# Kernel tuning notes

Measured on AMD Instinct MI355X. Metric: run time of the kernel, lower is better.

Reference implementation:

```python
import jax, jax.numpy as jnp
import numpy as np

B, C, H, W = 4, 256, 128, 128
HEADS = 8
EPS_LN = 1e-5
EPS_NORM = 1e-12


def conv2d(x, w, padding, groups=1):
    return jax.lax.conv_general_dilated(
        x, w, window_strides=(1, 1), padding=padding,
        feature_group_count=groups,
        dimension_numbers=('NCHW', 'OIHW', 'NCHW'))


def layernorm_c(x, weight, bias):
    # WithBias LayerNorm over channel dim (to_3d makes channels the last axis)
    mu = jnp.mean(x, axis=1, keepdims=True)
    var = jnp.var(x, axis=1, keepdims=True)
    xn = (x - mu) / jnp.sqrt(var + EPS_LN)
    return xn * weight[None, :, None, None] + bias[None, :, None, None]


def setup_inputs() -> dict:
    key = jax.random.key(0)
    ks = jax.random.split(key, 8)
    s = 0.02
    return {
        'x': jax.random.normal(ks[0], (B, C, H, W), jnp.float32),
        'y': jax.random.normal(ks[1], (B, C, H, W), jnp.float32),
        'ln_kv_w': jnp.ones((C,), jnp.float32),
        'ln_kv_b': jnp.zeros((C,), jnp.float32),
        'ln_q_w': jnp.ones((C,), jnp.float32),
        'ln_q_b': jnp.zeros((C,), jnp.float32),
        'W_kv': jax.random.normal(ks[2], (2 * C, C, 1, 1), jnp.float32) * s,
        'W_dw': jax.random.normal(ks[3], (2 * C, 1, 3, 3), jnp.float32) * s,
        'W_q': jax.random.normal(ks[4], (C, C, 3, 3), jnp.float32) * s,
        'W_proj': jax.random.normal(ks[5], (C, C, 1, 1), jnp.float32) * s,
        'temperature': jnp.ones((HEADS, 1, 1), jnp.float32),
    }


def reference(x, y, ln_kv_w, ln_kv_b, ln_q_w, ln_q_b, W_kv, W_dw, W_q, W_proj, temperature):
    b, c, h, w = x.shape
    xn = layernorm_c(x, ln_kv_w, ln_kv_b)
    yn = layernorm_c(y, ln_q_w, ln_q_b)

    # Attention (MDTA channel cross-attention)
    kv = conv2d(xn, W_kv, 'VALID')                       # [b, 2c, h, w]
    kv = conv2d(kv, W_dw, 'SAME', groups=2 * c)          # depthwise 3x3
    k, v = jnp.split(kv, 2, axis=1)
    q = conv2d(yn, W_q, 'SAME')                          # [b, c, h, w]

    def heads(t):
        return t.reshape(b, HEADS, c // HEADS, h * w)    # [b, head, ch, hw]

    q, k, v = heads(q), heads(k), heads(v)
    q = q / jnp.maximum(jnp.linalg.norm(q, axis=-1, keepdims=True), EPS_NORM)
    k = k / jnp.maximum(jnp.linalg.norm(k, axis=-1, keepdims=True), EPS_NORM)

    attn = jnp.einsum('bhcn,bhdn->bhcd', q, k) * temperature[None]
    attn = jax.nn.softmax(attn, axis=-1)
    out = jnp.einsum('bhcd,bhdn->bhcn', attn, v)         # [b, head, ch, hw]
    out = out.reshape(b, c, h, w)
    out = conv2d(out, W_proj, 'VALID')
    return yn + out
```

## Files before the change

kernel.cpp:

```cpp
#include <hip/hip_runtime.h>
#include <hip/hip_bf16.h>

typedef __hip_bfloat16 bf16;
typedef __attribute__((ext_vector_type(8))) short bf16x8;
typedef __attribute__((ext_vector_type(4))) float f32x4;

#define Bn 4
#define Cn 256
#define C2n 512
#define Hn 128
#define Wn 128
#define HWn 16384
#define HEADSn 8
#define CHn 32
#define PADW 132
#define PADH 130
#define PROW (PADW * Cn)
#define PBn ((size_t)PADH * PROW)

static __device__ __forceinline__ float b2f(bf16 v) { return __bfloat162float(v); }
static __device__ __forceinline__ bf16 f2b(float v) { return __float2bfloat16(v); }
static __device__ __forceinline__ short f2bs(float v) {
    bf16 t = f2b(v);
    return __builtin_bit_cast(short, t);
}
static __device__ __forceinline__ float s2f(short s) {
    bf16 t = __builtin_bit_cast(bf16, s);
    return b2f(t);
}

static __device__ __forceinline__ void gload16(const void* g, void* l) {
    __builtin_amdgcn_global_load_lds(
        (const __attribute__((address_space(1))) unsigned int*)g,
        (__attribute__((address_space(3))) unsigned int*)l,
        16, 0, 0);
}


__global__ void cast_kernel(const float* __restrict__ src, bf16* __restrict__ dst, int n) {
    for (int i = blockIdx.x * 256 + threadIdx.x; i < n; i += gridDim.x * 256)
        dst[i] = f2b(src[i]);
}

__global__ void wq_repack_kernel(const float* __restrict__ Wq, bf16* __restrict__ wr) {
    int i = blockIdx.x * 256 + threadIdx.x;
    if (i < Cn * Cn) {
        int oc = i >> 8, c = i & 255;
        #pragma unroll
        for (int dy = 0; dy < 3; dy++)
            #pragma unroll
            for (int dx = 0; dx < 3; dx++)
                wr[((size_t)dy * Cn + oc) * 768 + dx * Cn + c] =
                    f2b(Wq[(size_t)i * 9 + dy * 3 + dx]);
    }
}

__global__ void halo_zero_kernel(bf16* __restrict__ yp) {
    int yq = blockIdx.x;
    int b  = blockIdx.y;
    bf16* row = yp + (size_t)b * PBn + (size_t)yq * PROW;
    bf16x8 z = {0, 0, 0, 0, 0, 0, 0, 0};
    if (yq == 0 || yq == PADH - 1) {
        for (int i = threadIdx.x; i < PROW / 8; i += 256)
            *(bf16x8*)&row[(size_t)i * 8] = z;
    } else {
        for (int i = threadIdx.x; i < 128; i += 256) {
            if (i < 32) *(bf16x8*)&row[(size_t)i * 8] = z;
            else        *(bf16x8*)&row[(size_t)129 * Cn + (size_t)(i - 32) * 8] = z;
        }
    }
}

__global__ void ln_stats_kernel(const float* __restrict__ x,
                                const float* __restrict__ y,
                                float* __restrict__ stats) {
    int which = blockIdx.y;
    const float* src = which ? y : x;
    int pix = blockIdx.x * 256 + threadIdx.x;
    int b = pix >> 14;
    int hw = pix & (HWn - 1);
    const float* xb = src + (size_t)b * Cn * HWn + hw;
    float s = 0.f, ss = 0.f;
    for (int c = 0; c < Cn; c++) {
        float v = xb[(size_t)c * HWn];
        s += v; ss += v * v;
    }
    float mu  = s * (1.f / Cn);
    float var = ss * (1.f / Cn) - mu * mu;
    float inv = rsqrtf(var + 1e-5f);
    float* st = stats + (size_t)which * 2 * Bn * HWn;
    st[pix] = mu;
    st[(size_t)Bn * HWn + pix] = inv;
}

__global__ void transpose_ln_kernel(const float* __restrict__ src,
                                    const float* __restrict__ stats,
                                    const float* __restrict__ gw,
                                    const float* __restrict__ gb,
                                    bf16* __restrict__ dst, int pad) {
    __shared__ float t[64][65];
    __shared__ float swv[64], sbv[64], smu[64], sinv[64];
    int tid = threadIdx.x;
    int pxt = blockIdx.x;
    int ct  = blockIdx.y;
    int b   = blockIdx.z;
    int p0  = pxt * 64;
    if (tid < 64)       { swv[tid] = gw[ct * 64 + tid]; sbv[tid] = gb[ct * 64 + tid]; }
    else if (tid < 128) { int p = tid - 64;  smu[p]  = stats[(size_t)b * HWn + p0 + p]; }
    else if (tid < 192) { int p = tid - 128; sinv[p] = stats[(size_t)Bn * HWn + (size_t)b * HWn + p0 + p]; }
    const float* sb_ = src + ((size_t)b * Cn + ct * 64) * HWn + p0;
    for (int i = tid; i < 1024; i += 256) {
        int r = i >> 4, sg = (i & 15) * 4;
        float4 v = *(const float4*)&sb_[(size_t)r * HWn + sg];
        t[r][sg + 0] = v.x; t[r][sg + 1] = v.y; t[r][sg + 2] = v.z; t[r][sg + 3] = v.w;
    }
    __syncthreads();
    size_t base;
    if (pad) {
        int yr = p0 >> 7, x0 = p0 & 127;
        base = (size_t)b * PBn + ((size_t)(yr + 1) * PADW + (x0 + 1)) * Cn + ct * 64;
    } else {
        base = ((size_t)b * HWn + p0) * Cn + ct * 64;
    }
    for (int i = tid; i < 512; i += 256) {
        int p = i >> 3, cg = (i & 7) * 8;
        float mu = smu[p], inv = sinv[p];
        bf16x8 v;
        #pragma unroll
        for (int j = 0; j < 8; j++) {
            float val = (t[cg + j][p] - mu) * inv * swv[cg + j] + sbv[cg + j];
            v[j] = f2bs(val);
        }
        *(bf16x8*)&dst[base + (size_t)p * Cn + cg] = v;
    }
}

__global__ __launch_bounds__(256) void kv1x1_mfma_kernel(
        const bf16* __restrict__ xn_pm,
        const bf16* __restrict__ wkv_pk,
        bf16* __restrict__ kv) {
    __shared__ __attribute__((aligned(16))) short Als[8192];
    __shared__ __attribute__((aligned(16))) short Bls[8192];
    int tid  = threadIdx.x;
    int px0  = blockIdx.x * 128;
    int oc0  = blockIdx.y * 128;
    int b    = blockIdx.z;
    int wave = tid >> 6, lane = tid & 63;
    int lm = lane & 15, kq = lane >> 4;
    int l7 = lm & 7;

    f32x4 acc[2][8];
    #pragma unroll
    for (int mt = 0; mt < 2; mt++)
        #pragma unroll
        for (int nt = 0; nt < 8; nt++) acc[mt][nt] = (f32x4){0.f, 0.f, 0.f, 0.f};

    int rA = tid >> 3;
    int cA = (tid & 7) ^ (rA & 7);
    const short* pA = (const short*)wkv_pk + ((size_t)(oc0 + rA)) * Cn + cA * 8;
    const short* pB = (const short*)xn_pm + ((size_t)b * HWn + px0 + rA) * Cn + cA * 8;
    short* lA = &Als[wave * 512];
    short* lB = &Bls[wave * 512];

    for (int kc = 0; kc < Cn; kc += 64) {
        __syncthreads();
        #pragma unroll
        for (int j = 0; j < 4; j++) {
            gload16(pA + kc + j * (32 * Cn), lA + j * 2048);
            gload16(pB + kc + j * (32 * Cn), lB + j * 2048);
        }
        __syncthreads();
        #pragma unroll
        for (int kk = 0; kk < 2; kk++) {
            int xo = (((kk << 2) | kq) ^ l7) * 8;
            bf16x8 afr[2], bfr[8];
            #pragma unroll
            for (int mt = 0; mt < 2; mt++)
                afr[mt] = *(const bf16x8*)&Als[(wave * 32 + mt * 16 + lm) * 64 + xo];
            #pragma unroll
            for (int nt = 0; nt < 8; nt++)
                bfr[nt] = *(const bf16x8*)&Bls[(nt * 16 + lm) * 64 + xo];
            #pragma unroll
            for (int mt = 0; mt < 2; mt++)
                #pragma unroll
                for (int nt = 0; nt < 8; nt++)
                    acc[mt][nt] = __builtin_amdgcn_mfma_f32_16x16x32_bf16(
                        afr[mt], bfr[nt], acc[mt][nt], 0, 0, 0);
        }
    }
    bf16* kb = kv + ((size_t)b * C2n + oc0) * HWn + px0;
    #pragma unroll
    for (int mt = 0; mt < 2; mt++) {
        int ocl = wave * 32 + mt * 16 + kq * 4;
        #pragma unroll
        for (int nt = 0; nt < 8; nt++) {
            int pxx = nt * 16 + lm;
            #pragma unroll
            for (int r = 0; r < 4; r++)
                kb[(size_t)(ocl + r) * HWn + pxx] = f2b(acc[mt][nt][r]);
        }
    }
}

__global__ void dw_kernel(const bf16* __restrict__ kv,
                          const float* __restrict__ Wdw,
                          bf16* __restrict__ kvdw) {
    __shared__ float st[18][132];
    int tid = threadIdx.x;
    int r0  = blockIdx.x * 16;
    int ch  = blockIdx.y;
    int b   = blockIdx.z;
    float w[9];
    #pragma unroll
    for (int t = 0; t < 9; t++) w[t] = Wdw[ch * 9 + t];
    const bf16* base = kv + ((size_t)b * C2n + ch) * HWn;
    if (tid < 18) { st[tid][0] = 0.f; st[tid][129] = 0.f; }
    for (int i = tid; i < 288; i += 256) {
        int row = i >> 4, sg = (i & 15) << 3;
        int gr = r0 - 1 + row;
        bf16x8 v = {0, 0, 0, 0, 0, 0, 0, 0};
        if (gr >= 0 && gr < Hn) v = *(const bf16x8*)&base[(size_t)gr * Wn + sg];
        #pragma unroll
        for (int j = 0; j < 8; j++) st[row][1 + sg + j] = s2f(v[j]);
    }
    __syncthreads();
    int orow = tid >> 4, sg = (tid & 15) << 3;
    float o[8];
    #pragma unroll
    for (int j = 0; j < 8; j++) o[j] = 0.f;
    #pragma unroll
    for (int dy = 0; dy < 3; dy++)
        #pragma unroll
        for (int dx = 0; dx < 3; dx++) {
            float ww = w[dy * 3 + dx];
            #pragma unroll
            for (int j = 0; j < 8; j++) o[j] += ww * st[orow + dy][sg + j + dx];
        }
    bf16x8 ov;
    #pragma unroll
    for (int j = 0; j < 8; j++) ov[j] = f2bs(o[j]);
    *(bf16x8*)&kvdw[((size_t)b * C2n + ch) * HWn + (size_t)(r0 + orow) * Wn + sg] = ov;
}

__global__ __launch_bounds__(256, 2) void qconv_mfma_kernel(
        const bf16* __restrict__ ypad,
        const bf16* __restrict__ wq_r,
        bf16* __restrict__ q) {
    __shared__ __attribute__((aligned(16))) short Als[2][8192];
    __shared__ __attribute__((aligned(16))) short Bls[2][8192];
    int tid  = threadIdx.x;
    int xb_  = blockIdx.x;
    int y    = ((xb_ & 7) << 4) | (xb_ >> 3);
    int oc0  = blockIdx.y * 128;
    int b    = blockIdx.z;
    int wave = tid >> 6, lane = tid & 63;
    int lm = lane & 15, kq = lane >> 4;
    int l7 = lm & 7;

    f32x4 acc[2][8];
    #pragma unroll
    for (int mt = 0; mt < 2; mt++)
        #pragma unroll
        for (int nt = 0; nt < 8; nt++) acc[mt][nt] = (f32x4){0.f, 0.f, 0.f, 0.f};

    int rA = tid >> 3;
    int cA = (tid & 7) ^ (rA & 7);
    const short* pwA = (const short*)wq_r + ((size_t)(oc0 + rA)) * 768 + cA * 8;
    const short* pwB = (const short*)ypad + (size_t)b * PBn + (size_t)y * PROW
                     + (size_t)rA * Cn + cA * 8;
    int pk = 0;

#define STGQ(sel) { \
    short* la_ = &Als[sel][wave * 512]; \
    short* lb_ = &Bls[sel][wave * 512]; \
    _Pragma("unroll") \
    for (int j = 0; j < 4; j++) { \
        gload16(pwA + j * (32 * 768), la_ + j * 2048); \
        gload16(pwB + j * (32 * Cn),  lb_ + j * 2048); } }
#define BUMPQ() { \
    pk++; pwA += 64; pwB += 64; \
    if (pk == 12) { pk = 0; pwA += Cn * 768 - 768; pwB += PROW - 768; } }

    STGQ(0); BUMPQ();
    STGQ(1); BUMPQ();
    asm volatile("s_waitcnt vmcnt(8)" ::: "memory");
    __builtin_amdgcn_s_barrier();

    for (int t = 0; t < 36; t++) {
        int cur = t & 1;
        const short* Ab = &Als[cur][0];
        const short* Bb = &Bls[cur][0];
        bf16x8 afr[2][2], bfr[2][8];
        #pragma unroll
        for (int kk = 0; kk < 2; kk++) {
            int xo = (((kk << 2) | kq) ^ l7) * 8;
            #pragma unroll
            for (int mt = 0; mt < 2; mt++)
                afr[kk][mt] = *(const bf16x8*)&Ab[(wave * 32 + mt * 16 + lm) * 64 + xo];
            #pragma unroll
            for (int nt = 0; nt < 8; nt++)
                bfr[kk][nt] = *(const bf16x8*)&Bb[(nt * 16 + lm) * 64 + xo];
        }
        asm volatile("s_waitcnt lgkmcnt(0)" ::: "memory");
        __builtin_amdgcn_sched_barrier(0);
        __builtin_amdgcn_s_barrier();
        if (t < 34) { STGQ(cur); BUMPQ(); }
        #pragma unroll
        for (int kk = 0; kk < 2; kk++)
            #pragma unroll
            for (int mt = 0; mt < 2; mt++)
                #pragma unroll
                for (int nt = 0; nt < 8; nt++)
                    acc[mt][nt] = __builtin_amdgcn_mfma_f32_16x16x32_bf16(
                        afr[kk][mt], bfr[kk][nt], acc[mt][nt], 0, 0, 0);
        if (t < 34) asm volatile("s_waitcnt vmcnt(8)" ::: "memory");
        else        asm volatile("s_waitcnt vmcnt(0)" ::: "memory");
        __builtin_amdgcn_s_barrier();
    }
#undef STGQ
#undef BUMPQ
    bf16* qb = q + ((size_t)b * Cn + oc0) * HWn + (size_t)y * Wn;
    #pragma unroll
    for (int mt = 0; mt < 2; mt++) {
        int ocl = wave * 32 + mt * 16 + kq * 4;
        #pragma unroll
        for (int nt = 0; nt < 8; nt++) {
            int px = nt * 16 + lm;
            #pragma unroll
            for (int r = 0; r < 4; r++)
                qb[(size_t)(ocl + r) * HWn + px] = f2b(acc[mt][nt][r]);
        }
    }
}

__global__ __launch_bounds__(256) void attn_qk_kernel(
        const bf16* __restrict__ q,
        const bf16* __restrict__ kvdw,
        float* __restrict__ partial,
        float* __restrict__ qkp) {
    __shared__ short qls[32 * 264];
    __shared__ short kls[32 * 264];
    __shared__ float sred[4][1024];
    int tid   = threadIdx.x;
    int split = blockIdx.x;
    int bh    = blockIdx.y;
    int b = bh >> 3, h = bh & 7;
    int wave = tid >> 6, lane = tid & 63;
    int lm = lane & 15, kq = lane >> 4;

    const short* qbase = (const short*)(q    + ((size_t)(b * Cn  + h * CHn)) * HWn) + split * 2048;
    const short* kbase = (const short*)(kvdw + ((size_t)(b * C2n + h * CHn)) * HWn) + split * 2048;

    f32x4 acc[2][2];
    #pragma unroll
    for (int mt = 0; mt < 2; mt++)
        #pragma unroll
        for (int nt = 0; nt < 2; nt++) acc[mt][nt] = (f32x4){0.f, 0.f, 0.f, 0.f};

    float qss[4] = {0.f, 0.f, 0.f, 0.f};
    float kss[4] = {0.f, 0.f, 0.f, 0.f};
    int rb = tid >> 5, sgc = (tid & 31) * 8;

    for (int n0 = 0; n0 < 2048; n0 += 256) {
        __syncthreads();
        #pragma unroll
        for (int j = 0; j < 4; j++) {
            int r = rb + j * 8;
            bf16x8 qv = *(const bf16x8*)&qbase[(size_t)r * HWn + n0 + sgc];
            bf16x8 kv = *(const bf16x8*)&kbase[(size_t)r * HWn + n0 + sgc];
            *(bf16x8*)&qls[r * 264 + sgc] = qv;
            *(bf16x8*)&kls[r * 264 + sgc] = kv;
            #pragma unroll
            for (int e = 0; e < 8; e++) {
                float qf = s2f(qv[e]), kf = s2f(kv[e]);
                qss[j] += qf * qf;
                kss[j] += kf * kf;
            }
        }
        __syncthreads();
        int nb = wave * 64;
        #pragma unroll
        for (int kk = 0; kk < 64; kk += 32) {
            bf16x8 afr[2], bfr[2];
            #pragma unroll
            for (int mt = 0; mt < 2; mt++)
                afr[mt] = *(const bf16x8*)&qls[(mt * 16 + lm) * 264 + nb + kk + kq * 8];
            #pragma unroll
            for (int nt = 0; nt < 2; nt++)
                bfr[nt] = *(const bf16x8*)&kls[(nt * 16 + lm) * 264 + nb + kk + kq * 8];
            #pragma unroll
            for (int mt = 0; mt < 2; mt++)
                #pragma unroll
                for (int nt = 0; nt < 2; nt++)
                    acc[mt][nt] = __builtin_amdgcn_mfma_f32_16x16x32_bf16(
                        afr[mt], bfr[nt], acc[mt][nt], 0, 0, 0);
        }
    }
    __syncthreads();
    #pragma unroll
    for (int mt = 0; mt < 2; mt++)
        #pragma unroll
        for (int nt = 0; nt < 2; nt++)
            #pragma unroll
            for (int r = 0; r < 4; r++) {
                int c = mt * 16 + kq * 4 + r;
                int d = nt * 16 + lm;
                sred[wave][c * 32 + d] = acc[mt][nt][r];
            }
    #pragma unroll
    for (int off = 16; off > 0; off >>= 1) {
        #pragma unroll
        for (int j = 0; j < 4; j++) {
            qss[j] += __shfl_xor(qss[j], off);
            kss[j] += __shfl_xor(kss[j], off);
        }
    }
    if ((tid & 31) == 0) {
        float* qp = qkp + ((size_t)bh * 8 + split) * 64;
        #pragma unroll
        for (int j = 0; j < 4; j++) {
            qp[rb + 8 * j]      = qss[j];
            qp[32 + rb + 8 * j] = kss[j];
        }
    }
    __syncthreads();
    float* pb = partial + ((size_t)bh * 8 + split) * 1024;
    for (int i = tid; i < 1024; i += 256)
        pb[i] = sred[0][i] + sred[1][i] + sred[2][i] + sred[3][i];
}

__global__ void attn_softmax_kernel(const float* __restrict__ partial,
                                    const float* __restrict__ qkp,
                                    const float* __restrict__ temp,
                                    float* __restrict__ attn) {
    __shared__ float S[1024];
    __shared__ float sc[64];
    int bh = blockIdx.x;
    int h = bh & 7;
    int tid = threadIdx.x;
    if (tid < 64) {
        float s = 0.f;
        #pragma unroll
        for (int sp = 0; sp < 8; sp++)
            s += qkp[((size_t)bh * 8 + sp) * 64 + tid];
        sc[tid] = 1.f / fmaxf(sqrtf(s), 1e-12f);
    }
    __syncthreads();
    for (int i = tid; i < 1024; i += 256) {
        float v = 0.f;
        #pragma unroll
        for (int sp = 0; sp < 8; sp++)
            v += partial[((size_t)bh * 8 + sp) * 1024 + i];
        int c = i >> 5, d = i & 31;
        v *= sc[c] * sc[32 + d] * temp[h];
        S[i] = v;
    }
    __syncthreads();
    if (tid < 32) {
        int c = tid;
        float m = -1e30f;
        for (int d = 0; d < 32; d++) m = fmaxf(m, S[c * 32 + d]);
        float sum = 0.f;
        for (int d = 0; d < 32; d++) sum += __expf(S[c * 32 + d] - m);
        float inv = 1.f / sum;
        for (int d = 0; d < 32; d++)
            attn[(size_t)bh * 1024 + c * 32 + d] = __expf(S[c * 32 + d] - m) * inv;
    }
}

__global__ void av_kernel(const float* __restrict__ attn,
                          const bf16* __restrict__ kvdw,
                          bf16* __restrict__ ao_pm) {
    int bh = blockIdx.y;
    int b = bh >> 3, h = bh & 7;
    int tid = threadIdx.x;
    int n = blockIdx.x * 256 + tid;
    __shared__ float At[32][32];
    for (int i = tid; i < 1024; i += 256) {
        int cc = i >> 5, dd = i & 31;
        At[dd][cc] = attn[((size_t)bh * 32 + cc) * 32 + dd];
    }
    __syncthreads();
    const bf16* vbase = kvdw + ((size_t)b * C2n + Cn + h * CHn) * HWn;
    float acc[32];
    #pragma unroll
    for (int c = 0; c < 32; c++) acc[c] = 0.f;
    for (int d = 0; d < 32; d++) {
        float vv = b2f(vbase[(size_t)d * HWn + n]);
        #pragma unroll
        for (int c = 0; c < 32; c++) acc[c] += At[d][c] * vv;
    }
    bf16* obase = ao_pm + ((size_t)b * HWn + n) * Cn + h * CHn;
    #pragma unroll
    for (int g = 0; g < 4; g++) {
        bf16x8 v;
        #pragma unroll
        for (int j = 0; j < 8; j++) v[j] = f2bs(acc[g * 8 + j]);
        *(bf16x8*)&obase[g * 8] = v;
    }
}

__global__ __launch_bounds__(256) void proj_mfma_kernel(
        const bf16* __restrict__ ao_pm,
        const bf16* __restrict__ wpr_pk,
        const bf16* __restrict__ ypad,
        float* __restrict__ out) {
    __shared__ __attribute__((aligned(16))) short Als[8192];
    __shared__ __attribute__((aligned(16))) short Bls[8192];
    int tid  = threadIdx.x;
    int y    = blockIdx.x;
    int px0  = y * 128;
    int oc0  = blockIdx.y * 128;
    int b    = blockIdx.z;
    int wave = tid >> 6, lane = tid & 63;
    int lm = lane & 15, kq = lane >> 4;
    int l7 = lm & 7;

    f32x4 acc[2][8];
    #pragma unroll
    for (int mt = 0; mt < 2; mt++)
        #pragma unroll
        for (int nt = 0; nt < 8; nt++) acc[mt][nt] = (f32x4){0.f, 0.f, 0.f, 0.f};

    int rA = tid >> 3;
    int cA = (tid & 7) ^ (rA & 7);
    const short* pA = (const short*)wpr_pk + ((size_t)(oc0 + rA)) * Cn + cA * 8;
    const short* pB = (const short*)ao_pm + ((size_t)b * HWn + px0 + rA) * Cn + cA * 8;
    short* lA = &Als[wave * 512];
    short* lB = &Bls[wave * 512];

    for (int kc = 0; kc < Cn; kc += 64) {
        __syncthreads();
        #pragma unroll
        for (int j = 0; j < 4; j++) {
            gload16(pA + kc + j * (32 * Cn), lA + j * 2048);
            gload16(pB + kc + j * (32 * Cn), lB + j * 2048);
        }
        __syncthreads();
        #pragma unroll
        for (int kk = 0; kk < 2; kk++) {
            int xo = (((kk << 2) | kq) ^ l7) * 8;
            bf16x8 afr[2], bfr[8];
            #pragma unroll
            for (int mt = 0; mt < 2; mt++)
                afr[mt] = *(const bf16x8*)&Als[(wave * 32 + mt * 16 + lm) * 64 + xo];
            #pragma unroll
            for (int nt = 0; nt < 8; nt++)
                bfr[nt] = *(const bf16x8*)&Bls[(nt * 16 + lm) * 64 + xo];
            #pragma unroll
            for (int mt = 0; mt < 2; mt++)
                #pragma unroll
                for (int nt = 0; nt < 8; nt++)
                    acc[mt][nt] = __builtin_amdgcn_mfma_f32_16x16x32_bf16(
                        afr[mt], bfr[nt], acc[mt][nt], 0, 0, 0);
        }
    }
    const short* ynp = (const short*)ypad + (size_t)b * PBn
                     + ((size_t)(y + 1) * PADW + 1) * Cn;
    float* ob = out + ((size_t)b * Cn + oc0) * HWn + px0;
    #pragma unroll
    for (int mt = 0; mt < 2; mt++) {
        int ocl = wave * 32 + mt * 16 + kq * 4;
        #pragma unroll
        for (int nt = 0; nt < 8; nt++) {
            int px = nt * 16 + lm;
            #pragma unroll
            for (int r = 0; r < 4; r++)
                ob[(size_t)(ocl + r) * HWn + px] =
                    acc[mt][nt][r] + s2f(ynp[(size_t)px * Cn + oc0 + ocl + r]);
        }
    }
}

extern "C" void kernel_launch(void* const* d_in, const int* in_sizes, int n_in,
                              void* d_out, int out_size, void* d_ws, size_t ws_size,
                              hipStream_t stream) {
    const float* x     = (const float*)d_in[0];
    const float* y     = (const float*)d_in[1];
    const float* lnkw  = (const float*)d_in[2];
    const float* lnkb  = (const float*)d_in[3];
    const float* lnqw  = (const float*)d_in[4];
    const float* lnqb  = (const float*)d_in[5];
    const float* Wkv   = (const float*)d_in[6];
    const float* Wdw   = (const float*)d_in[7];
    const float* Wq    = (const float*)d_in[8];
    const float* Wproj = (const float*)d_in[9];
    const float* temp  = (const float*)d_in[10];
    float* out = (float*)d_out;

    char* ws = (char*)d_ws;
    const size_t TENB = (size_t)Bn * Cn * HWn * 2;
    bf16* kvb   = (bf16*)ws;
    bf16* q_cm  = (bf16*)ws;
    bf16* kvdw  = (bf16*)(ws + 2 * TENB);
    bf16*  xn_pm = (bf16*)(ws + 4 * TENB);
    bf16*  ao_pm = xn_pm;
    float* partS = (float*)(ws + 4 * TENB);
    bf16* yn_pad = (bf16*)(ws + 5 * TENB);
    char* wp = ws + 5 * TENB + (size_t)Bn * PBn * 2;
    bf16* wq_r   = (bf16*)wp;  wp += (size_t)3 * Cn * 768 * 2;
    bf16* wkv_pk = (bf16*)wp;  wp += (size_t)C2n * Cn * 2;
    bf16* wpr_pk = (bf16*)wp;  wp += (size_t)Cn * Cn * 2;
    float* qkp   = (float*)wp; wp += 65536;
    float* attnP = (float*)wp; wp += 131072;
    float* stats = (float*)wp; wp += (size_t)2 * 2 * Bn * HWn * 4;

    wq_repack_kernel<<<dim3(256), 256, 0, stream>>>(Wq, wq_r);
    cast_kernel<<<dim3(128), 256, 0, stream>>>(Wkv, wkv_pk, C2n * Cn);
    cast_kernel<<<dim3(64), 256, 0, stream>>>(Wproj, wpr_pk, Cn * Cn);
    halo_zero_kernel<<<dim3(PADH, Bn), 256, 0, stream>>>(yn_pad);
    ln_stats_kernel<<<dim3(Bn * HWn / 256, 2), 256, 0, stream>>>(x, y, stats);
    transpose_ln_kernel<<<dim3(HWn / 64, Cn / 64, Bn), 256, 0, stream>>>(
        x, stats, lnkw, lnkb, xn_pm, 0);
    transpose_ln_kernel<<<dim3(HWn / 64, Cn / 64, Bn), 256, 0, stream>>>(
        y, stats + (size_t)2 * Bn * HWn, lnqw, lnqb, yn_pad, 1);
    kv1x1_mfma_kernel<<<dim3(HWn / 128, C2n / 128, Bn), 256, 0, stream>>>(xn_pm, wkv_pk, kvb);
    dw_kernel<<<dim3(Hn / 16, C2n, Bn), 256, 0, stream>>>(kvb, Wdw, kvdw);
    qconv_mfma_kernel<<<dim3(Hn, Cn / 128, Bn), 256, 0, stream>>>(yn_pad, wq_r, q_cm);
    attn_qk_kernel<<<dim3(8, Bn * HEADSn), 256, 0, stream>>>(q_cm, kvdw, partS, qkp);
    attn_softmax_kernel<<<dim3(Bn * HEADSn), 256, 0, stream>>>(partS, qkp, temp, attnP);
    av_kernel<<<dim3(HWn / 256, Bn * HEADSn), 256, 0, stream>>>(attnP, kvdw, ao_pm);
    proj_mfma_kernel<<<dim3(HWn / 128, Cn / 128, Bn), 256, 0, stream>>>(ao_pm, wpr_pk, yn_pad, out);
}
```

Measured before the change: 470.9 us.

## Fuse LayerNorm stats into transpose kernel and double-buffer 1x1 GEMM K-loop

```diff
diff --git a/kernel.cpp b/kernel.cpp
--- a/kernel.cpp
+++ b/kernel.cpp
@@ -71,76 +71,70 @@
     }
 }
 
-__global__ void ln_stats_kernel(const float* __restrict__ x,
-                                const float* __restrict__ y,
-                                float* __restrict__ stats) {
-    int which = blockIdx.y;
-    const float* src = which ? y : x;
-    int pix = blockIdx.x * 256 + threadIdx.x;
-    int b = pix >> 14;
-    int hw = pix & (HWn - 1);
-    const float* xb = src + (size_t)b * Cn * HWn + hw;
-    float s = 0.f, ss = 0.f;
-    for (int c = 0; c < Cn; c++) {
-        float v = xb[(size_t)c * HWn];
-        s += v; ss += v * v;
-    }
-    float mu  = s * (1.f / Cn);
-    float var = ss * (1.f / Cn) - mu * mu;
-    float inv = rsqrtf(var + 1e-5f);
-    float* st = stats + (size_t)which * 2 * Bn * HWn;
-    st[pix] = mu;
-    st[(size_t)Bn * HWn + pix] = inv;
-}
-
-__global__ void transpose_ln_kernel(const float* __restrict__ src,
-                                    const float* __restrict__ stats,
-                                    const float* __restrict__ gw,
-                                    const float* __restrict__ gb,
-                                    bf16* __restrict__ dst, int pad) {
-    __shared__ float t[64][65];
-    __shared__ float swv[64], sbv[64], smu[64], sinv[64];
+__global__ __launch_bounds__(256) void lnt_kernel(
+        const float* __restrict__ src,
+        const float* __restrict__ gw,
+        const float* __restrict__ gb,
+        bf16* __restrict__ dst, int pad) {
+    __shared__ float t[256][65];
+    __shared__ float sw[256], sb[256];
+    __shared__ float red_s[4][64], red_ss[4][64];
+    __shared__ float smu[64], sinv[64];
     int tid = threadIdx.x;
     int pxt = blockIdx.x;
-    int ct  = blockIdx.y;
-    int b   = blockIdx.z;
+    int b   = blockIdx.y;
     int p0  = pxt * 64;
-    if (tid < 64)       { swv[tid] = gw[ct * 64 + tid]; sbv[tid] = gb[ct * 64 + tid]; }
-    else if (tid < 128) { int p = tid - 64;  smu[p]  = stats[(size_t)b * HWn + p0 + p]; }
-    else if (tid < 192) { int p = tid - 128; sinv[p] = stats[(size_t)Bn * HWn + (size_t)b * HWn + p0 + p]; }
-    const float* sb_ = src + ((size_t)b * Cn + ct * 64) * HWn + p0;
-    for (int i = tid; i < 1024; i += 256) {
+    sw[tid] = gw[tid]; sb[tid] = gb[tid];
+    const float* sb_ = src + (size_t)b * Cn * HWn + p0;
+    for (int i = tid; i < 4096; i += 256) {
         int r = i >> 4, sg = (i & 15) * 4;
         float4 v = *(const float4*)&sb_[(size_t)r * HWn + sg];
-        t[r][sg + 0] = v.x; t[r][sg + 1] = v.y; t[r][sg + 2] = v.z; t[r][sg + 3] = v.w;
+        t[r][sg] = v.x; t[r][sg + 1] = v.y; t[r][sg + 2] = v.z; t[r][sg + 3] = v.w;
+    }
+    __syncthreads();
+    {
+        int px = tid & 63, q = tid >> 6;
+        float s = 0.f, ss = 0.f;
+        int c0 = q * 64;
+        for (int c = c0; c < c0 + 64; c++) {
+            float v = t[c][px];
+            s += v; ss += v * v;
+        }
+        red_s[q][px] = s; red_ss[q][px] = ss;
+    }
+    __syncthreads();
+    if (tid < 64) {
+        float s  = red_s[0][tid] + red_s[1][tid] + red_s[2][tid] + red_s[3][tid];
+        float ss = red_ss[0][tid] + red_ss[1][tid] + red_ss[2][tid] + red_ss[3][tid];
+        float mu  = s * (1.f / Cn);
+        float var = ss * (1.f / Cn) - mu * mu;
+        smu[tid] = mu; sinv[tid] = rsqrtf(var + 1e-5f);
     }
     __syncthreads();
     size_t base;
     if (pad) {
         int yr = p0 >> 7, x0 = p0 & 127;
-        base = (size_t)b * PBn + ((size_t)(yr + 1) * PADW + (x0 + 1)) * Cn + ct * 64;
+        base = (size_t)b * PBn + ((size_t)(yr + 1) * PADW + (x0 + 1)) * Cn;
     } else {
-        base = ((size_t)b * HWn + p0) * Cn + ct * 64;
-    }
-    for (int i = tid; i < 512; i += 256) {
-        int p = i >> 3, cg = (i & 7) * 8;
-        float mu = smu[p], inv = sinv[p];
+        base = ((size_t)b * HWn + p0) * Cn;
+    }
+    for (int i = tid; i < 2048; i += 256) {
+        int px = i >> 5, cg = (i & 31) * 8;
+        float mu = smu[px], inv = sinv[px];
         bf16x8 v;
         #pragma unroll
-        for (int j = 0; j < 8; j++) {
-            float val = (t[cg + j][p] - mu) * inv * swv[cg + j] + sbv[cg + j];
-            v[j] = f2bs(val);
-        }
-        *(bf16x8*)&dst[base + (size_t)p * Cn + cg] = v;
-    }
-}
-
-__global__ __launch_bounds__(256) void kv1x1_mfma_kernel(
+        for (int j = 0; j < 8; j++)
+            v[j] = f2bs((t[cg + j][px] - mu) * inv * sw[cg + j] + sb[cg + j]);
+        *(bf16x8*)&dst[base + (size_t)px * Cn + cg] = v;
+    }
+}
+
+__global__ __launch_bounds__(256, 2) void kv1x1_mfma_kernel(
         const bf16* __restrict__ xn_pm,
         const bf16* __restrict__ wkv_pk,
         bf16* __restrict__ kv) {
-    __shared__ __attribute__((aligned(16))) short Als[8192];
-    __shared__ __attribute__((aligned(16))) short Bls[8192];
+    __shared__ __attribute__((aligned(16))) short Als[2][8192];
+    __shared__ __attribute__((aligned(16))) short Bls[2][8192];
     int tid  = threadIdx.x;
     int px0  = blockIdx.x * 128;
     int oc0  = blockIdx.y * 128;
@@ -159,35 +153,52 @@
     int cA = (tid & 7) ^ (rA & 7);
     const short* pA = (const short*)wkv_pk + ((size_t)(oc0 + rA)) * Cn + cA * 8;
     const short* pB = (const short*)xn_pm + ((size_t)b * HWn + px0 + rA) * Cn + cA * 8;
-    short* lA = &Als[wave * 512];
-    short* lB = &Bls[wave * 512];
-
-    for (int kc = 0; kc < Cn; kc += 64) {
-        __syncthreads();
-        #pragma unroll
-        for (int j = 0; j < 4; j++) {
-            gload16(pA + kc + j * (32 * Cn), lA + j * 2048);
-            gload16(pB + kc + j * (32 * Cn), lB + j * 2048);
-        }
-        __syncthreads();
+
+#define STG1(sel) { \
+    short* la_ = &Als[sel][wave * 512]; \
+    short* lb_ = &Bls[sel][wave * 512]; \
+    _Pragma("unroll") \
+    for (int j = 0; j < 4; j++) { \
+        gload16(pA + j * (32 * Cn), la_ + j * 2048); \
+        gload16(pB + j * (32 * Cn), lb_ + j * 2048); } }
+
+    STG1(0); pA += 64; pB += 64;
+    STG1(1); pA += 64; pB += 64;
+    asm volatile("s_waitcnt vmcnt(8)" ::: "memory");
+    __builtin_amdgcn_s_barrier();
+
+    for (int t = 0; t < 4; t++) {
+        int cur = t & 1;
+        const short* Ab = &Als[cur][0];
+        const short* Bb = &Bls[cur][0];
+        bf16x8 afr[2][2], bfr[2][8];
         #pragma unroll
         for (int kk = 0; kk < 2; kk++) {
             int xo = (((kk << 2) | kq) ^ l7) * 8;
-            bf16x8 afr[2], bfr[8];
-            #pragma unroll
-            for (int mt = 0; mt < 2; mt++)
-                afr[mt] = *(const bf16x8*)&Als[(wave * 32 + mt * 16 + lm) * 64 + xo];
+            #pragma unroll
+            for (int mt = 0; mt < 2; mt++)
+                afr[kk][mt] = *(const bf16x8*)&Ab[(wave * 32 + mt * 16 + lm) * 64 + xo];
             #pragma unroll
             for (int nt = 0; nt < 8; nt++)
-                bfr[nt] = *(const bf16x8*)&Bls[(nt * 16 + lm) * 64 + xo];
+                bfr[kk][nt] = *(const bf16x8*)&Bb[(nt * 16 + lm) * 64 + xo];
+        }
+        asm volatile("s_waitcnt lgkmcnt(0)" ::: "memory");
+        __builtin_amdgcn_sched_barrier(0);
+        __builtin_amdgcn_s_barrier();
+        if (t < 2) { STG1(cur); pA += 64; pB += 64; }
+        #pragma unroll
+        for (int kk = 0; kk < 2; kk++)
             #pragma unroll
             for (int mt = 0; mt < 2; mt++)
                 #pragma unroll
                 for (int nt = 0; nt < 8; nt++)
                     acc[mt][nt] = __builtin_amdgcn_mfma_f32_16x16x32_bf16(
-                        afr[mt], bfr[nt], acc[mt][nt], 0, 0, 0);
-        }
-    }
+                        afr[kk][mt], bfr[kk][nt], acc[mt][nt], 0, 0, 0);
+        if (t < 2) asm volatile("s_waitcnt vmcnt(8)" ::: "memory");
+        else       asm volatile("s_waitcnt vmcnt(0)" ::: "memory");
+        __builtin_amdgcn_s_barrier();
+    }
+#undef STG1
     bf16* kb = kv + ((size_t)b * C2n + oc0) * HWn + px0;
     #pragma unroll
     for (int mt = 0; mt < 2; mt++) {
@@ -500,13 +511,13 @@
     }
 }
 
-__global__ __launch_bounds__(256) void proj_mfma_kernel(
+__global__ __launch_bounds__(256, 2) void proj_mfma_kernel(
         const bf16* __restrict__ ao_pm,
         const bf16* __restrict__ wpr_pk,
         const bf16* __restrict__ ypad,
         float* __restrict__ out) {
-    __shared__ __attribute__((aligned(16))) short Als[8192];
-    __shared__ __attribute__((aligned(16))) short Bls[8192];
+    __shared__ __attribute__((aligned(16))) short Als[2][8192];
+    __shared__ __attribute__((aligned(16))) short Bls[2][8192];
     int tid  = threadIdx.x;
     int y    = blockIdx.x;
     int px0  = y * 128;
@@ -526,35 +537,52 @@
     int cA = (tid & 7) ^ (rA & 7);
     const short* pA = (const short*)wpr_pk + ((size_t)(oc0 + rA)) * Cn + cA * 8;
     const short* pB = (const short*)ao_pm + ((size_t)b * HWn + px0 + rA) * Cn + cA * 8;
-    short* lA = &Als[wave * 512];
-    short* lB = &Bls[wave * 512];
-
-    for (int kc = 0; kc < Cn; kc += 64) {
-        __syncthreads();
-        #pragma unroll
-        for (int j = 0; j < 4; j++) {
-            gload16(pA + kc + j * (32 * Cn), lA + j * 2048);
-            gload16(pB + kc + j * (32 * Cn), lB + j * 2048);
-        }
-        __syncthreads();
+
+#define STGP(sel) { \
+    short* la_ = &Als[sel][wave * 512]; \
+    short* lb_ = &Bls[sel][wave * 512]; \
+    _Pragma("unroll") \
+    for (int j = 0; j < 4; j++) { \
+        gload16(pA + j * (32 * Cn), la_ + j * 2048); \
+        gload16(pB + j * (32 * Cn), lb_ + j * 2048); } }
+
+    STGP(0); pA += 64; pB += 64;
+    STGP(1); pA += 64; pB += 64;
+    asm volatile("s_waitcnt vmcnt(8)" ::: "memory");
+    __builtin_amdgcn_s_barrier();
+
+    for (int t = 0; t < 4; t++) {
+        int cur = t & 1;
+        const short* Ab = &Als[cur][0];
+        const short* Bb = &Bls[cur][0];
+        bf16x8 afr[2][2], bfr[2][8];
         #pragma unroll
         for (int kk = 0; kk < 2; kk++) {
             int xo = (((kk << 2) | kq) ^ l7) * 8;
-            bf16x8 afr[2], bfr[8];
-            #pragma unroll
-            for (int mt = 0; mt < 2; mt++)
-                afr[mt] = *(const bf16x8*)&Als[(wave * 32 + mt * 16 + lm) * 64 + xo];
+            #pragma unroll
+            for (int mt = 0; mt < 2; mt++)
+                afr[kk][mt] = *(const bf16x8*)&Ab[(wave * 32 + mt * 16 + lm) * 64 + xo];
             #pragma unroll
             for (int nt = 0; nt < 8; nt++)
-                bfr[nt] = *(const bf16x8*)&Bls[(nt * 16 + lm) * 64 + xo];
+                bfr[kk][nt] = *(const bf16x8*)&Bb[(nt * 16 + lm) * 64 + xo];
+        }
+        asm volatile("s_waitcnt lgkmcnt(0)" ::: "memory");
+        __builtin_amdgcn_sched_barrier(0);
+        __builtin_amdgcn_s_barrier();
+        if (t < 2) { STGP(cur); pA += 64; pB += 64; }
+        #pragma unroll
+        for (int kk = 0; kk < 2; kk++)
             #pragma unroll
             for (int mt = 0; mt < 2; mt++)
                 #pragma unroll
                 for (int nt = 0; nt < 8; nt++)
                     acc[mt][nt] = __builtin_amdgcn_mfma_f32_16x16x32_bf16(
-                        afr[mt], bfr[nt], acc[mt][nt], 0, 0, 0);
-        }
-    }
+                        afr[kk][mt], bfr[kk][nt], acc[mt][nt], 0, 0, 0);
+        if (t < 2) asm volatile("s_waitcnt vmcnt(8)" ::: "memory");
+        else       asm volatile("s_waitcnt vmcnt(0)" ::: "memory");
+        __builtin_amdgcn_s_barrier();
+    }
+#undef STGP
     const short* ynp = (const short*)ypad + (size_t)b * PBn
                      + ((size_t)(y + 1) * PADW + 1) * Cn;
     float* ob = out + ((size_t)b * Cn + oc0) * HWn + px0;
@@ -603,17 +631,13 @@
     bf16* wpr_pk = (bf16*)wp;  wp += (size_t)Cn * Cn * 2;
     float* qkp   = (float*)wp; wp += 65536;
     float* attnP = (float*)wp; wp += 131072;
-    float* stats = (float*)wp; wp += (size_t)2 * 2 * Bn * HWn * 4;
 
     wq_repack_kernel<<<dim3(256), 256, 0, stream>>>(Wq, wq_r);
     cast_kernel<<<dim3(128), 256, 0, stream>>>(Wkv, wkv_pk, C2n * Cn);
     cast_kernel<<<dim3(64), 256, 0, stream>>>(Wproj, wpr_pk, Cn * Cn);
     halo_zero_kernel<<<dim3(PADH, Bn), 256, 0, stream>>>(yn_pad);
-    ln_stats_kernel<<<dim3(Bn * HWn / 256, 2), 256, 0, stream>>>(x, y, stats);
-    transpose_ln_kernel<<<dim3(HWn / 64, Cn / 64, Bn), 256, 0, stream>>>(
-        x, stats, lnkw, lnkb, xn_pm, 0);
-    transpose_ln_kernel<<<dim3(HWn / 64, Cn / 64, Bn), 256, 0, stream>>>(
-        y, stats + (size_t)2 * Bn * HWn, lnqw, lnqb, yn_pad, 1);
+    lnt_kernel<<<dim3(HWn / 64, Bn), 256, 0, stream>>>(x, lnkw, lnkb, xn_pm, 0);
+    lnt_kernel<<<dim3(HWn / 64, Bn), 256, 0, stream>>>(y, lnqw, lnqb, yn_pad, 1);
     kv1x1_mfma_kernel<<<dim3(HWn / 128, C2n / 128, Bn), 256, 0, stream>>>(xn_pm, wkv_pk, kvb);
     dw_kernel<<<dim3(Hn / 16, C2n, Bn), 256, 0, stream>>>(kvb, Wdw, kvdw);
     qconv_mfma_kernel<<<dim3(Hn, Cn / 128, Bn), 256, 0, stream>>>(yn_pad, wq_r, q_cm);
```

Result: faster. 424.7 us (-9.8%).
